# Kernel tuning notes

Measured on AMD Instinct MI355X. Metric: run time of the kernel, lower is better.

## Reference

```python
import jax, jax.numpy as jnp
import numpy as np

N = 50000
E = 800000
F_IN = 128
LN_EPS = 1e-5
NEG_SLOPE = 0.2


def _add_self_loops(edge_index, n):
    loop = jnp.arange(n, dtype=edge_index.dtype)
    src = jnp.concatenate([edge_index[0], loop])
    dst = jnp.concatenate([edge_index[1], loop])
    return src, dst


def gat_conv(x, src, dst, W, att_src, att_dst, bias, heads, ch, concat):
    """PyG GATConv (eval mode, add_self_loops already applied via src/dst)."""
    n = x.shape[0]
    h = (x @ W).reshape(n, heads, ch)                       # [N,H,C]
    a_s = (h * att_src[None]).sum(-1)                       # [N,H]
    a_d = (h * att_dst[None]).sum(-1)                       # [N,H]
    alpha = jax.nn.leaky_relu(a_s[src] + a_d[dst], NEG_SLOPE)  # [E,H]
    # segment softmax over incoming edges of each destination node
    amax = jax.ops.segment_max(alpha, dst, num_segments=n)
    amax = jnp.where(jnp.isfinite(amax), amax, 0.0)
    alpha = jnp.exp(alpha - amax[dst])
    denom = jax.ops.segment_sum(alpha, dst, num_segments=n)
    alpha = alpha / (denom[dst] + 1e-16)
    msg = h[src] * alpha[:, :, None]                        # [E,H,C]
    out = jax.ops.segment_sum(msg, dst, num_segments=n)     # [N,H,C]
    if concat:
        out = out.reshape(n, heads * ch)
    else:
        out = out.mean(axis=1)
    return out + bias


def layer_norm(x, g, b):
    mu = x.mean(-1, keepdims=True)
    var = ((x - mu) ** 2).mean(-1, keepdims=True)
    return (x - mu) * jax.lax.rsqrt(var + LN_EPS) * g + b


def setup_inputs() -> dict:
    key = jax.random.key(0)
    ks = jax.random.split(key, 12)
    x = jax.random.normal(ks[0], (N, F_IN), jnp.float32)
    edge_index = jax.random.randint(ks[1], (2, E), 0, N, dtype=jnp.int64)

    def glorot(k, shape, fan_in):
        return jax.random.normal(k, shape, jnp.float32) / np.sqrt(fan_in)

    return {
        "x": x,
        "edge_index": edge_index,
        # conv1: 128 -> 64, heads=2, concat -> 128
        "W1": glorot(ks[2], (F_IN, 2 * 64), F_IN),
        "as1": glorot(ks[3], (2, 64), 64),
        "ad1": glorot(ks[4], (2, 64), 64),
        "b1": jnp.zeros((128,), jnp.float32),
        "g1": jnp.ones((128,), jnp.float32),
        "be1": jnp.zeros((128,), jnp.float32),
        # conv2: 128 -> 32, heads=2, concat -> 64
        "W2": glorot(ks[5], (128, 2 * 32), 128),
        "as2": glorot(ks[6], (2, 32), 32),
        "ad2": glorot(ks[7], (2, 32), 32),
        "b2": jnp.zeros((64,), jnp.float32),
        "g2": jnp.ones((64,), jnp.float32),
        "be2": jnp.zeros((64,), jnp.float32),
        # conv3: 64 -> 2, heads=1
        "W3": glorot(ks[8], (64, 2), 64),
        "as3": glorot(ks[9], (1, 2), 2),
        "ad3": glorot(ks[10], (1, 2), 2),
        "b3": jnp.zeros((2,), jnp.float32),
    }


def reference(x, edge_index, W1, as1, ad1, b1, g1, be1,
              W2, as2, ad2, b2, g2, be2, W3, as3, ad3, b3):
    src, dst = _add_self_loops(edge_index, x.shape[0])
    h = gat_conv(x, src, dst, W1, as1, ad1, b1, heads=2, ch=64, concat=True)
    h = jax.nn.elu(layer_norm(h, g1, be1))
    h = gat_conv(h, src, dst, W2, as2, ad2, b2, heads=2, ch=32, concat=True)
    h = jax.nn.elu(layer_norm(h, g2, be2))
    h = gat_conv(h, src, dst, W3, as3, ad3, b3, heads=1, ch=2, concat=True)
    return jax.nn.log_softmax(h, axis=1)
```

## Files before the change

kernel.cpp:

```cpp
#include <hip/hip_runtime.h>
#include <hip/hip_fp16.h>
#include <math.h>

#define LN_EPS 1e-5f
#define NEG_SLOPE 0.2f
#define CAP 128
#define CNT_STRIDE 32

__global__ void scatter_pad(const int* __restrict__ ei, int E, int N,
                            int* __restrict__ cnt, int* __restrict__ col) {
    int T = E + N;
    int stride = gridDim.x * blockDim.x;
    int e = blockIdx.x * blockDim.x + threadIdx.x;
    bool ok[4];
    int s[4], d[4], pos[4];
#pragma unroll
    for (int u = 0; u < 4; ++u) {
        int ee = e + u * stride;
        ok[u] = (ee < T);
        int ec = ok[u] ? ee : 0;
        s[u] = (ec < E) ? ei[ec] : (ec - E);
        d[u] = (ec < E) ? ei[E + ec] : (ec - E);
    }
#pragma unroll
    for (int u = 0; u < 4; ++u) {
        if (ok[u]) pos[u] = atomicAdd(&cnt[(size_t)d[u] * CNT_STRIDE], 1);
    }
#pragma unroll
    for (int u = 0; u < 4; ++u) {
        if (ok[u] && pos[u] < CAP) col[(size_t)d[u] * CAP + pos[u]] = s[u];
    }
}

template <int K, int M>
__launch_bounds__(256)
__global__ void gemm_att(const float* __restrict__ X, const float* __restrict__ W,
                         const float* __restrict__ AS, const float* __restrict__ AD,
                         __half* __restrict__ Yh, float* __restrict__ a_s,
                         float* __restrict__ a_d, int N) {
    constexpr int BR = 64, CT = 4, RT = 8, KC = 64;
    constexpr int TC = M / CT;
    constexpr int NT = TC * (BR / RT);
    constexpr int HG = TC / 2;
    __shared__ float Xs[BR][KC];
    __shared__ float Ws[KC][M];
    int tid = threadIdx.x;
    if (tid >= NT) return;
    int tc = tid % TC, tr = tid / TC;
    int row0 = blockIdx.x * BR;
    float acc[RT][CT] = {};
#pragma unroll
    for (int kc = 0; kc < K; kc += KC) {
        constexpr int XV = (BR * KC / 4) / NT;
#pragma unroll
        for (int i = 0; i < XV; ++i) {
            int f = tid + i * NT;
            int r = f / (KC / 4), c4 = f % (KC / 4);
            int row = row0 + r;
            float4 v = (row < N) ? *reinterpret_cast<const float4*>(&X[(size_t)row * K + kc + c4 * 4])
                                 : make_float4(0.f, 0.f, 0.f, 0.f);
            *reinterpret_cast<float4*>(&Xs[r][c4 * 4]) = v;
        }
        constexpr int WV = (KC * M / 4) / NT;
#pragma unroll
        for (int i = 0; i < WV; ++i) {
            int f = tid + i * NT;
            int kk = f / (M / 4), c4 = f % (M / 4);
            *reinterpret_cast<float4*>(&Ws[kk][c4 * 4]) =
                *reinterpret_cast<const float4*>(&W[(size_t)(kc + kk) * M + c4 * 4]);
        }
        __syncthreads();
#pragma unroll 4
        for (int k = 0; k < KC; ++k) {
            float4 wv = *reinterpret_cast<const float4*>(&Ws[k][tc * 4]);
#pragma unroll
            for (int rr = 0; rr < RT; ++rr) {
                float xv = Xs[tr * RT + rr][k];
                acc[rr][0] += xv * wv.x;
                acc[rr][1] += xv * wv.y;
                acc[rr][2] += xv * wv.z;
                acc[rr][3] += xv * wv.w;
            }
        }
        __syncthreads();
    }
    float4 asv = *reinterpret_cast<const float4*>(&AS[tc * 4]);
    float4 adv = *reinterpret_cast<const float4*>(&AD[tc * 4]);
#pragma unroll
    for (int rr = 0; rr < RT; ++rr) {
        int row = row0 + tr * RT + rr;
        if (row < N) {
            union { __half2 h[2]; uint2 u; } pk;
            pk.h[0] = __floats2half2_rn(acc[rr][0], acc[rr][1]);
            pk.h[1] = __floats2half2_rn(acc[rr][2], acc[rr][3]);
            *reinterpret_cast<uint2*>(&Yh[(size_t)row * M + tc * 4]) = pk.u;
        }
        float ps = acc[rr][0] * asv.x + acc[rr][1] * asv.y + acc[rr][2] * asv.z + acc[rr][3] * asv.w;
        float pd = acc[rr][0] * adv.x + acc[rr][1] * adv.y + acc[rr][2] * adv.z + acc[rr][3] * adv.w;
#pragma unroll
        for (int off = 1; off < HG; off <<= 1) {
            ps += __shfl_xor(ps, off);
            pd += __shfl_xor(pd, off);
        }
        if ((tc & (HG - 1)) == 0 && row < N) {
            int head = tc / HG;
            a_s[row * 2 + head] = ps;
            a_d[row * 2 + head] = pd;
        }
    }
}

__launch_bounds__(256)
__global__ void l3_transform(const float* __restrict__ X, const float* __restrict__ W3,
                             const float* __restrict__ as3, const float* __restrict__ ad3,
                             __half* __restrict__ h3h, float* __restrict__ a_s,
                             float* __restrict__ a_d, int N) {
    int n = blockIdx.x * blockDim.x + threadIdx.x;
    if (n >= N) return;
    const float4* xp = reinterpret_cast<const float4*>(&X[(size_t)n * 64]);
    float h0 = 0.f, h1 = 0.f;
#pragma unroll
    for (int i = 0; i < 16; ++i) {
        float4 x4 = xp[i];
        int k = i * 4;
        h0 += x4.x * W3[(k + 0) * 2] + x4.y * W3[(k + 1) * 2] +
              x4.z * W3[(k + 2) * 2] + x4.w * W3[(k + 3) * 2];
        h1 += x4.x * W3[(k + 0) * 2 + 1] + x4.y * W3[(k + 1) * 2 + 1] +
              x4.z * W3[(k + 2) * 2 + 1] + x4.w * W3[(k + 3) * 2 + 1];
    }
    *reinterpret_cast<__half2*>(&h3h[(size_t)n * 2]) = __floats2half2_rn(h0, h1);
    a_s[n] = h0 * as3[0] + h1 * as3[1];
    a_d[n] = h0 * ad3[0] + h1 * ad3[1];
}

template <int HH, int C, int MODE>
__launch_bounds__(256)
__global__ void gat_gather(const int* __restrict__ col,
                           const int* __restrict__ cnt, const __half* __restrict__ Hf,
                           const float* __restrict__ a_s, const float* __restrict__ a_d,
                           const float* __restrict__ bias, const float* __restrict__ gw,
                           const float* __restrict__ bw, float* __restrict__ outp, int N) {
    int wid = blockIdx.x * (blockDim.x >> 6) + (threadIdx.x >> 6);
    int lane = threadIdx.x & 63;
    if (wid >= N) return;
    const int d = wid;
    const size_t start = (size_t)d * CAP;
    const int deg = cnt[(size_t)d * CNT_STRIDE];

    if constexpr (MODE == 1) {
        float ad0 = a_d[d];
        float m0 = -INFINITY, s0 = 0.f, acc0 = 0.f, acc1 = 0.f;
        if (deg <= 64) {
            int src_l = (lane < deg) ? col[start + lane] : 0;
            float lg0 = -INFINITY;
            if (lane < deg) {
                float v0 = a_s[src_l] + ad0;
                lg0 = (v0 > 0.f) ? v0 : NEG_SLOPE * v0;
            }
            m0 = lg0;
#pragma unroll
            for (int off = 32; off > 0; off >>= 1) m0 = fmaxf(m0, __shfl_xor(m0, off));
            float e0 = 0.f;
            if (lane < deg) {
                e0 = __expf(lg0 - m0);
                float2 f = __half22float2(*reinterpret_cast<const __half2*>(Hf + (size_t)src_l * 2));
                acc0 = e0 * f.x;
                acc1 = e0 * f.y;
            }
            s0 = e0;
#pragma unroll
            for (int off = 32; off > 0; off >>= 1) {
                s0 += __shfl_xor(s0, off);
                acc0 += __shfl_xor(acc0, off);
                acc1 += __shfl_xor(acc1, off);
            }
        } else {
            for (int base = 0; base < deg; base += 64) {
                int j = base + lane;
                if (j < deg) {
                    int src = col[start + j];
                    float v0 = a_s[src] + ad0;
                    v0 = (v0 > 0.f) ? v0 : NEG_SLOPE * v0;
                    float nm = fmaxf(m0, v0);
                    float sc = (m0 == -INFINITY) ? 0.f : __expf(m0 - nm);
                    float e = __expf(v0 - nm);
                    float2 f = __half22float2(*reinterpret_cast<const __half2*>(Hf + (size_t)src * 2));
                    s0 = s0 * sc + e;
                    acc0 = acc0 * sc + e * f.x;
                    acc1 = acc1 * sc + e * f.y;
                    m0 = nm;
                }
            }
#pragma unroll
            for (int off = 32; off > 0; off >>= 1) {
                float om = __shfl_xor(m0, off);
                float os = __shfl_xor(s0, off);
                float oa0 = __shfl_xor(acc0, off);
                float oa1 = __shfl_xor(acc1, off);
                float nm = fmaxf(m0, om);
                float t1 = (m0 == -INFINITY) ? 0.f : __expf(m0 - nm);
                float t2 = (om == -INFINITY) ? 0.f : __expf(om - nm);
                m0 = nm;
                s0 = s0 * t1 + os * t2;
                acc0 = acc0 * t1 + oa0 * t2;
                acc1 = acc1 * t1 + oa1 * t2;
            }
        }
        if (lane == 0) {
            float inv = 1.f / (s0 + 1e-16f);
            float h0 = acc0 * inv + bias[0];
            float h1 = acc1 * inv + bias[1];
            float mx = fmaxf(h0, h1);
            float l = mx + logf(expf(h0 - mx) + expf(h1 - mx));
            *reinterpret_cast<float2*>(outp + (size_t)d * 2) = make_float2(h0 - l, h1 - l);
        }
    }

    if constexpr (MODE == 0) {
        constexpr int M = HH * C;
        constexpr int FPL = (M / 64 > 0) ? (M / 64) : 1;
        __shared__ int   s_src[4][64];
        __shared__ float s_cf[4][2][64];
        const int wslot = (threadIdx.x >> 6);
        const int t0 = lane * FPL;
        const int hl = lane >> 5;

        float ad0 = a_d[d * 2];
        float ad1 = a_d[d * 2 + 1];

        float acc[FPL] = {};

        if (deg <= 64) {
            int src_l = (lane < deg) ? col[start + lane] : 0;
            float lg0 = -INFINITY, lg1 = -INFINITY;
            if (lane < deg) {
                float2 av = *reinterpret_cast<const float2*>(a_s + (size_t)src_l * 2);
                float v0 = av.x + ad0;
                lg0 = (v0 > 0.f) ? v0 : NEG_SLOPE * v0;
                float v1 = av.y + ad1;
                lg1 = (v1 > 0.f) ? v1 : NEG_SLOPE * v1;
            }
            float m0 = lg0, m1 = lg1;
#pragma unroll
            for (int off = 32; off > 0; off >>= 1) {
                m0 = fmaxf(m0, __shfl_xor(m0, off));
                m1 = fmaxf(m1, __shfl_xor(m1, off));
            }
            float e0 = (lane < deg) ? __expf(lg0 - m0) : 0.f;
            float e1 = (lane < deg) ? __expf(lg1 - m1) : 0.f;
            float s0 = e0, s1 = e1;
#pragma unroll
            for (int off = 32; off > 0; off >>= 1) {
                s0 += __shfl_xor(s0, off);
                s1 += __shfl_xor(s1, off);
            }
            float inv0 = 1.f / (s0 + 1e-16f);
            float inv1 = 1.f / (s1 + 1e-16f);
            s_src[wslot][lane] = src_l;
            s_cf[wslot][0][lane] = e0 * inv0;
            s_cf[wslot][1][lane] = e1 * inv1;

            const float* cp = &s_cf[wslot][hl][0];
            const int* sp = &s_src[wslot][0];
            int j = 0;
            for (; j + 4 <= deg; j += 4) {
                int i0 = sp[j], i1 = sp[j + 1], i2 = sp[j + 2], i3 = sp[j + 3];
                float c0 = cp[j], c1 = cp[j + 1], c2 = cp[j + 2], c3 = cp[j + 3];
                if constexpr (FPL == 2) {
                    __half2 r0 = *reinterpret_cast<const __half2*>(Hf + (size_t)i0 * M + t0);
                    __half2 r1 = *reinterpret_cast<const __half2*>(Hf + (size_t)i1 * M + t0);
                    __half2 r2 = *reinterpret_cast<const __half2*>(Hf + (size_t)i2 * M + t0);
                    __half2 r3 = *reinterpret_cast<const __half2*>(Hf + (size_t)i3 * M + t0);
                    float2 f0 = __half22float2(r0), f1 = __half22float2(r1);
                    float2 f2 = __half22float2(r2), f3 = __half22float2(r3);
                    acc[0] += c0 * f0.x + c1 * f1.x + c2 * f2.x + c3 * f3.x;
                    acc[1] += c0 * f0.y + c1 * f1.y + c2 * f2.y + c3 * f3.y;
                } else {
                    float f0 = __half2float(Hf[(size_t)i0 * M + t0]);
                    float f1 = __half2float(Hf[(size_t)i1 * M + t0]);
                    float f2 = __half2float(Hf[(size_t)i2 * M + t0]);
                    float f3 = __half2float(Hf[(size_t)i3 * M + t0]);
                    acc[0] += c0 * f0 + c1 * f1 + c2 * f2 + c3 * f3;
                }
            }
            for (; j < deg; ++j) {
                int i0 = sp[j];
                float c0 = cp[j];
                if constexpr (FPL == 2) {
                    float2 f0 = __half22float2(*reinterpret_cast<const __half2*>(Hf + (size_t)i0 * M + t0));
                    acc[0] += c0 * f0.x;
                    acc[1] += c0 * f0.y;
                } else {
                    acc[0] += c0 * __half2float(Hf[(size_t)i0 * M + t0]);
                }
            }
        } else {
            float m0 = -INFINITY, m1 = -INFINITY, s0 = 0.f, s1 = 0.f;
            for (int base = 0; base < deg; base += 64) {
                int j = base + lane;
                if (j < deg) {
                    int src = col[start + j];
                    float2 av = *reinterpret_cast<const float2*>(a_s + (size_t)src * 2);
                    float v0 = av.x + ad0;
                    v0 = (v0 > 0.f) ? v0 : NEG_SLOPE * v0;
                    float nm = fmaxf(m0, v0);
                    s0 = s0 * ((m0 == -INFINITY) ? 0.f : __expf(m0 - nm)) + __expf(v0 - nm);
                    m0 = nm;
                    float v1 = av.y + ad1;
                    v1 = (v1 > 0.f) ? v1 : NEG_SLOPE * v1;
                    float nm1 = fmaxf(m1, v1);
                    s1 = s1 * ((m1 == -INFINITY) ? 0.f : __expf(m1 - nm1)) + __expf(v1 - nm1);
                    m1 = nm1;
                }
            }
#pragma unroll
            for (int off = 32; off > 0; off >>= 1) {
                float om = __shfl_xor(m0, off);
                float os = __shfl_xor(s0, off);
                float nm = fmaxf(m0, om);
                float t1 = (m0 == -INFINITY) ? 0.f : __expf(m0 - nm);
                float t2 = (om == -INFINITY) ? 0.f : __expf(om - nm);
                m0 = nm;
                s0 = s0 * t1 + os * t2;
                float om1 = __shfl_xor(m1, off);
                float os1 = __shfl_xor(s1, off);
                float nm1 = fmaxf(m1, om1);
                float u1 = (m1 == -INFINITY) ? 0.f : __expf(m1 - nm1);
                float u2 = (om1 == -INFINITY) ? 0.f : __expf(om1 - nm1);
                m1 = nm1;
                s1 = s1 * u1 + os1 * u2;
            }
            float inv0 = 1.f / (s0 + 1e-16f);
            float inv1 = 1.f / (s1 + 1e-16f);
            for (int base = 0; base < deg; base += 64) {
                int rem = deg - base;
                int nchunk = (rem < 64) ? rem : 64;
                int j = base + lane;
                int src_l = (lane < nchunk) ? col[start + j] : 0;
                float e0 = 0.f, e1 = 0.f;
                if (lane < nchunk) {
                    float2 av = *reinterpret_cast<const float2*>(a_s + (size_t)src_l * 2);
                    float v0 = av.x + ad0;
                    v0 = (v0 > 0.f) ? v0 : NEG_SLOPE * v0;
                    e0 = __expf(v0 - m0) * inv0;
                    float v1 = av.y + ad1;
                    v1 = (v1 > 0.f) ? v1 : NEG_SLOPE * v1;
                    e1 = __expf(v1 - m1) * inv1;
                }
                s_src[wslot][lane] = src_l;
                s_cf[wslot][0][lane] = e0;
                s_cf[wslot][1][lane] = e1;
                const float* cp = &s_cf[wslot][hl][0];
                const int* sp = &s_src[wslot][0];
                int jj = 0;
                for (; jj + 4 <= nchunk; jj += 4) {
                    int i0 = sp[jj], i1 = sp[jj + 1], i2 = sp[jj + 2], i3 = sp[jj + 3];
                    float c0 = cp[jj], c1 = cp[jj + 1], c2 = cp[jj + 2], c3 = cp[jj + 3];
                    if constexpr (FPL == 2) {
                        __half2 r0 = *reinterpret_cast<const __half2*>(Hf + (size_t)i0 * M + t0);
                        __half2 r1 = *reinterpret_cast<const __half2*>(Hf + (size_t)i1 * M + t0);
                        __half2 r2 = *reinterpret_cast<const __half2*>(Hf + (size_t)i2 * M + t0);
                        __half2 r3 = *reinterpret_cast<const __half2*>(Hf + (size_t)i3 * M + t0);
                        float2 f0 = __half22float2(r0), f1 = __half22float2(r1);
                        float2 f2 = __half22float2(r2), f3 = __half22float2(r3);
                        acc[0] += c0 * f0.x + c1 * f1.x + c2 * f2.x + c3 * f3.x;
                        acc[1] += c0 * f0.y + c1 * f1.y + c2 * f2.y + c3 * f3.y;
                    } else {
                        float f0 = __half2float(Hf[(size_t)i0 * M + t0]);
                        float f1 = __half2float(Hf[(size_t)i1 * M + t0]);
                        float f2 = __half2float(Hf[(size_t)i2 * M + t0]);
                        float f3 = __half2float(Hf[(size_t)i3 * M + t0]);
                        acc[0] += c0 * f0 + c1 * f1 + c2 * f2 + c3 * f3;
                    }
                }
                for (; jj < nchunk; ++jj) {
                    int i0 = sp[jj];
                    float c0 = cp[jj];
                    if constexpr (FPL == 2) {
                        float2 f0 = __half22float2(*reinterpret_cast<const __half2*>(Hf + (size_t)i0 * M + t0));
                        acc[0] += c0 * f0.x;
                        acc[1] += c0 * f0.y;
                    } else {
                        acc[0] += c0 * __half2float(Hf[(size_t)i0 * M + t0]);
                    }
                }
            }
        }

        float v[FPL];
        float ls = 0.f;
#pragma unroll
        for (int jj = 0; jj < FPL; ++jj) {
            v[jj] = acc[jj] + bias[t0 + jj];
            ls += v[jj];
        }
#pragma unroll
        for (int off = 32; off > 0; off >>= 1) ls += __shfl_xor(ls, off);
        float mu = ls * (1.0f / M);
        float lv = 0.f;
#pragma unroll
        for (int jj = 0; jj < FPL; ++jj) {
            float dv = v[jj] - mu;
            lv += dv * dv;
        }
#pragma unroll
        for (int off = 32; off > 0; off >>= 1) lv += __shfl_xor(lv, off);
        float rstd = rsqrtf(lv * (1.0f / M) + LN_EPS);
#pragma unroll
        for (int jj = 0; jj < FPL; ++jj) {
            float y = (v[jj] - mu) * rstd * gw[t0 + jj] + bw[t0 + jj];
            v[jj] = (y > 0.f) ? y : expm1f(y);
        }
        if constexpr (FPL == 2) {
            *reinterpret_cast<float2*>(outp + (size_t)d * M + t0) = make_float2(v[0], v[1]);
        } else {
            outp[(size_t)d * M + t0] = v[0];
        }
    }
}

extern "C" void kernel_launch(void* const* d_in, const int* in_sizes, int n_in,
                              void* d_out, int out_size, void* d_ws, size_t ws_size,
                              hipStream_t stream) {
    const float* x   = (const float*)d_in[0];
    const int*   ei  = (const int*)d_in[1];
    const float* W1  = (const float*)d_in[2];
    const float* as1 = (const float*)d_in[3];
    const float* ad1 = (const float*)d_in[4];
    const float* b1  = (const float*)d_in[5];
    const float* g1  = (const float*)d_in[6];
    const float* be1 = (const float*)d_in[7];
    const float* W2  = (const float*)d_in[8];
    const float* as2 = (const float*)d_in[9];
    const float* ad2 = (const float*)d_in[10];
    const float* b2  = (const float*)d_in[11];
    const float* g2  = (const float*)d_in[12];
    const float* be2 = (const float*)d_in[13];
    const float* W3  = (const float*)d_in[14];
    const float* as3 = (const float*)d_in[15];
    const float* ad3 = (const float*)d_in[16];
    const float* b3  = (const float*)d_in[17];

    int N = in_sizes[0] / 128;
    int E = in_sizes[1] / 2;
    int T = E + N;

    __half* Hh  = (__half*)d_ws;
    float* feat = (float*)(Hh + (size_t)N * 128);
    float* a_s  = feat + (size_t)N * 128;
    float* a_d  = a_s + (size_t)N * 2;
    int* cnt    = (int*)(a_d + (size_t)N * 2);
    int* col    = cnt + (size_t)N * CNT_STRIDE;

    (void)hipMemsetAsync(cnt, 0, (size_t)N * CNT_STRIDE * sizeof(int), stream);
    int ublocks = (T + 1023) / 1024;
    scatter_pad<<<ublocks, 256, 0, stream>>>(ei, E, N, cnt, col);

    int gblocks = (N + 3) / 4;
    int rblocks = (N + 63) / 64;

    gemm_att<128, 128><<<rblocks, 256, 0, stream>>>(x, W1, as1, ad1, Hh, a_s, a_d, N);
    gat_gather<2, 64, 0><<<gblocks, 256, 0, stream>>>(col, cnt, Hh, a_s, a_d,
                                                      b1, g1, be1, feat, N);

    gemm_att<128, 64><<<rblocks, 128, 0, stream>>>(feat, W2, as2, ad2, Hh, a_s, a_d, N);
    gat_gather<2, 32, 0><<<gblocks, 256, 0, stream>>>(col, cnt, Hh, a_s, a_d,
                                                      b2, g2, be2, feat, N);

    l3_transform<<<(N + 255) / 256, 256, 0, stream>>>(feat, W3, as3, ad3, Hh, a_s, a_d, N);
    gat_gather<1, 2, 1><<<gblocks, 256, 0, stream>>>(col, cnt, Hh, a_s, a_d,
                                                     b3, nullptr, nullptr, (float*)d_out, N);
}
```

Before: 217.6 us.

## Fuse layer-3 transform into layer-2 gather epilogue and scalarize gather indices

The separate l3_transform kernel is removed. Its 64->2 projection and attention logits are now computed in the epilogue of the layer-2 gather via a wave reduction, which avoids writing and re-reading the layer-2 feature matrix and saves one kernel launch. Separate buffers are added for the layer-3 outputs. In addition, the neighbor indices and coefficients read from shared memory are broadcast with readfirstlane so they can live in scalar registers. This adds a select per coefficient depending on the head half.

Result: slower. 242.9 us (+11.6%).

```diff
diff --git a/kernel.cpp b/kernel.cpp
--- a/kernel.cpp
+++ b/kernel.cpp
@@ -6,6 +6,11 @@
 #define NEG_SLOPE 0.2f
 #define CAP 128
 #define CNT_STRIDE 32
+
+__device__ inline int rfl_i(int x) { return __builtin_amdgcn_readfirstlane(x); }
+__device__ inline float rfl_f(float x) {
+    return __uint_as_float(__builtin_amdgcn_readfirstlane(__float_as_uint(x)));
+}
 
 __global__ void scatter_pad(const int* __restrict__ ei, int E, int N,
                             int* __restrict__ cnt, int* __restrict__ col) {
@@ -110,36 +115,16 @@
     }
 }
 
-__launch_bounds__(256)
-__global__ void l3_transform(const float* __restrict__ X, const float* __restrict__ W3,
-                             const float* __restrict__ as3, const float* __restrict__ ad3,
-                             __half* __restrict__ h3h, float* __restrict__ a_s,
-                             float* __restrict__ a_d, int N) {
-    int n = blockIdx.x * blockDim.x + threadIdx.x;
-    if (n >= N) return;
-    const float4* xp = reinterpret_cast<const float4*>(&X[(size_t)n * 64]);
-    float h0 = 0.f, h1 = 0.f;
-#pragma unroll
-    for (int i = 0; i < 16; ++i) {
-        float4 x4 = xp[i];
-        int k = i * 4;
-        h0 += x4.x * W3[(k + 0) * 2] + x4.y * W3[(k + 1) * 2] +
-              x4.z * W3[(k + 2) * 2] + x4.w * W3[(k + 3) * 2];
-        h1 += x4.x * W3[(k + 0) * 2 + 1] + x4.y * W3[(k + 1) * 2 + 1] +
-              x4.z * W3[(k + 2) * 2 + 1] + x4.w * W3[(k + 3) * 2 + 1];
-    }
-    *reinterpret_cast<__half2*>(&h3h[(size_t)n * 2]) = __floats2half2_rn(h0, h1);
-    a_s[n] = h0 * as3[0] + h1 * as3[1];
-    a_d[n] = h0 * ad3[0] + h1 * ad3[1];
-}
-
 template <int HH, int C, int MODE>
 __launch_bounds__(256)
 __global__ void gat_gather(const int* __restrict__ col,
                            const int* __restrict__ cnt, const __half* __restrict__ Hf,
                            const float* __restrict__ a_s, const float* __restrict__ a_d,
                            const float* __restrict__ bias, const float* __restrict__ gw,
-                           const float* __restrict__ bw, float* __restrict__ outp, int N) {
+                           const float* __restrict__ bw, float* __restrict__ outp, int N,
+                           const float* __restrict__ W3p, const float* __restrict__ as3p,
+                           const float* __restrict__ ad3p, __half* __restrict__ h3p,
+                           float* __restrict__ as3o, float* __restrict__ ad3o) {
     int wid = blockIdx.x * (blockDim.x >> 6) + (threadIdx.x >> 6);
     int lane = threadIdx.x & 63;
     if (wid >= N) return;
@@ -216,7 +201,7 @@
         }
     }
 
-    if constexpr (MODE == 0) {
+    if constexpr (MODE == 0 || MODE == 2) {
         constexpr int M = HH * C;
         constexpr int FPL = (M / 64 > 0) ? (M / 64) : 1;
         __shared__ int   s_src[4][64];
@@ -260,12 +245,17 @@
             s_cf[wslot][0][lane] = e0 * inv0;
             s_cf[wslot][1][lane] = e1 * inv1;
 
-            const float* cp = &s_cf[wslot][hl][0];
+            const float* cp0 = &s_cf[wslot][0][0];
+            const float* cp1 = &s_cf[wslot][1][0];
             const int* sp = &s_src[wslot][0];
             int j = 0;
             for (; j + 4 <= deg; j += 4) {
-                int i0 = sp[j], i1 = sp[j + 1], i2 = sp[j + 2], i3 = sp[j + 3];
-                float c0 = cp[j], c1 = cp[j + 1], c2 = cp[j + 2], c3 = cp[j + 3];
+                int i0 = rfl_i(sp[j]), i1 = rfl_i(sp[j + 1]);
+                int i2 = rfl_i(sp[j + 2]), i3 = rfl_i(sp[j + 3]);
+                float c0 = (hl == 0) ? rfl_f(cp0[j]) : rfl_f(cp1[j]);
+                float c1 = (hl == 0) ? rfl_f(cp0[j + 1]) : rfl_f(cp1[j + 1]);
+                float c2 = (hl == 0) ? rfl_f(cp0[j + 2]) : rfl_f(cp1[j + 2]);
+                float c3 = (hl == 0) ? rfl_f(cp0[j + 3]) : rfl_f(cp1[j + 3]);
                 if constexpr (FPL == 2) {
                     __half2 r0 = *reinterpret_cast<const __half2*>(Hf + (size_t)i0 * M + t0);
                     __half2 r1 = *reinterpret_cast<const __half2*>(Hf + (size_t)i1 * M + t0);
@@ -284,8 +274,8 @@
                 }
             }
             for (; j < deg; ++j) {
-                int i0 = sp[j];
-                float c0 = cp[j];
+                int i0 = rfl_i(sp[j]);
+                float c0 = (hl == 0) ? rfl_f(cp0[j]) : rfl_f(cp1[j]);
                 if constexpr (FPL == 2) {
                     float2 f0 = __half22float2(*reinterpret_cast<const __half2*>(Hf + (size_t)i0 * M + t0));
                     acc[0] += c0 * f0.x;
@@ -350,12 +340,17 @@
                 s_src[wslot][lane] = src_l;
                 s_cf[wslot][0][lane] = e0;
                 s_cf[wslot][1][lane] = e1;
-                const float* cp = &s_cf[wslot][hl][0];
+                const float* cp0 = &s_cf[wslot][0][0];
+                const float* cp1 = &s_cf[wslot][1][0];
                 const int* sp = &s_src[wslot][0];
                 int jj = 0;
                 for (; jj + 4 <= nchunk; jj += 4) {
-                    int i0 = sp[jj], i1 = sp[jj + 1], i2 = sp[jj + 2], i3 = sp[jj + 3];
-                    float c0 = cp[jj], c1 = cp[jj + 1], c2 = cp[jj + 2], c3 = cp[jj + 3];
+                    int i0 = rfl_i(sp[jj]), i1 = rfl_i(sp[jj + 1]);
+                    int i2 = rfl_i(sp[jj + 2]), i3 = rfl_i(sp[jj + 3]);
+                    float c0 = (hl == 0) ? rfl_f(cp0[jj]) : rfl_f(cp1[jj]);
+                    float c1 = (hl == 0) ? rfl_f(cp0[jj + 1]) : rfl_f(cp1[jj + 1]);
+                    float c2 = (hl == 0) ? rfl_f(cp0[jj + 2]) : rfl_f(cp1[jj + 2]);
+                    float c3 = (hl == 0) ? rfl_f(cp0[jj + 3]) : rfl_f(cp1[jj + 3]);
                     if constexpr (FPL == 2) {
                         __half2 r0 = *reinterpret_cast<const __half2*>(Hf + (size_t)i0 * M + t0);
                         __half2 r1 = *reinterpret_cast<const __half2*>(Hf + (size_t)i1 * M + t0);
@@ -374,8 +369,8 @@
                     }
                 }
                 for (; jj < nchunk; ++jj) {
-                    int i0 = sp[jj];
-                    float c0 = cp[jj];
+                    int i0 = rfl_i(sp[jj]);
+                    float c0 = (hl == 0) ? rfl_f(cp0[jj]) : rfl_f(cp1[jj]);
                     if constexpr (FPL == 2) {
                         float2 f0 = __half22float2(*reinterpret_cast<const __half2*>(Hf + (size_t)i0 * M + t0));
                         acc[0] += c0 * f0.x;
@@ -411,10 +406,27 @@
             float y = (v[jj] - mu) * rstd * gw[t0 + jj] + bw[t0 + jj];
             v[jj] = (y > 0.f) ? y : expm1f(y);
         }
-        if constexpr (FPL == 2) {
-            *reinterpret_cast<float2*>(outp + (size_t)d * M + t0) = make_float2(v[0], v[1]);
+
+        if constexpr (MODE == 0) {
+            if constexpr (FPL == 2) {
+                *reinterpret_cast<float2*>(outp + (size_t)d * M + t0) = make_float2(v[0], v[1]);
+            } else {
+                outp[(size_t)d * M + t0] = v[0];
+            }
         } else {
-            outp[(size_t)d * M + t0] = v[0];
+            float2 w = *reinterpret_cast<const float2*>(W3p + t0 * 2);
+            float h0 = v[0] * w.x;
+            float h1 = v[0] * w.y;
+#pragma unroll
+            for (int off = 32; off > 0; off >>= 1) {
+                h0 += __shfl_xor(h0, off);
+                h1 += __shfl_xor(h1, off);
+            }
+            if (lane == 0) {
+                *reinterpret_cast<__half2*>(h3p + (size_t)d * 2) = __floats2half2_rn(h0, h1);
+                as3o[d] = h0 * as3p[0] + h1 * as3p[1];
+                ad3o[d] = h0 * ad3p[0] + h1 * ad3p[1];
+            }
         }
     }
 }
@@ -449,25 +461,33 @@
     float* feat = (float*)(Hh + (size_t)N * 128);
     float* a_s  = feat + (size_t)N * 128;
     float* a_d  = a_s + (size_t)N * 2;
-    int* cnt    = (int*)(a_d + (size_t)N * 2);
+    float* a_s3 = a_d + (size_t)N * 2;
+    float* a_d3 = a_s3 + (size_t)N;
+    __half* h3  = (__half*)(a_d3 + (size_t)N);
+    int* cnt    = (int*)(h3 + (size_t)N * 2);
     int* col    = cnt + (size_t)N * CNT_STRIDE;
 
     (void)hipMemsetAsync(cnt, 0, (size_t)N * CNT_STRIDE * sizeof(int), stream);
+
     int ublocks = (T + 1023) / 1024;
-    scatter_pad<<<ublocks, 256, 0, stream>>>(ei, E, N, cnt, col);
-
     int gblocks = (N + 3) / 4;
     int rblocks = (N + 63) / 64;
 
+    scatter_pad<<<ublocks, 256, 0, stream>>>(ei, E, N, cnt, col);
+
     gemm_att<128, 128><<<rblocks, 256, 0, stream>>>(x, W1, as1, ad1, Hh, a_s, a_d, N);
     gat_gather<2, 64, 0><<<gblocks, 256, 0, stream>>>(col, cnt, Hh, a_s, a_d,
-                                                      b1, g1, be1, feat, N);
+                                                      b1, g1, be1, feat, N,
+                                                      nullptr, nullptr, nullptr, nullptr,
+                                                      nullptr, nullptr);
 
     gemm_att<128, 64><<<rblocks, 128, 0, stream>>>(feat, W2, as2, ad2, Hh, a_s, a_d, N);
-    gat_gather<2, 32, 0><<<gblocks, 256, 0, stream>>>(col, cnt, Hh, a_s, a_d,
-                                                      b2, g2, be2, feat, N);
-
-    l3_transform<<<(N + 255) / 256, 256, 0, stream>>>(feat, W3, as3, ad3, Hh, a_s, a_d, N);
-    gat_gather<1, 2, 1><<<gblocks, 256, 0, stream>>>(col, cnt, Hh, a_s, a_d,
-                                                     b3, nullptr, nullptr, (float*)d_out, N);
+    gat_gather<2, 32, 2><<<gblocks, 256, 0, stream>>>(col, cnt, Hh, a_s, a_d,
+                                                      b2, g2, be2, nullptr, N,
+                                                      W3, as3, ad3, h3, a_s3, a_d3);
+
+    gat_gather<1, 2, 1><<<gblocks, 256, 0, stream>>>(col, cnt, h3, a_s3, a_d3,
+                                                     b3, nullptr, nullptr, (float*)d_out, N,
+                                                     nullptr, nullptr, nullptr, nullptr,
+                                                     nullptr, nullptr);
 }
```
